# Optimization experiments

Measured on AMD Instinct MI355X. Metric: run time of the kernel, lower is better.

## Reference

```python
import jax, jax.numpy as jnp
import numpy as np

# Config (decoder-only Transformer)
NL, H, D, DK, V, B, S = 6, 16, 1024, 64, 32000, 2, 1024  # DK = d_v = D // H
DFF = 4 * D


def _layer_norm(x, g, b, eps=1e-5):
    mu = jnp.mean(x, axis=-1, keepdims=True)
    var = jnp.mean(jnp.square(x - mu), axis=-1, keepdims=True)
    return (x - mu) * jax.lax.rsqrt(var + eps) * g + b


def _pos_encoding(seq_len, d_embed):
    # Matches PositionalEncoding: base 1000 (as in source), sin at even i, cos at odd i
    pos = jnp.arange(seq_len, dtype=jnp.float32)[:, None]
    i = jnp.arange(d_embed, dtype=jnp.float32)[None, :]
    angle = pos / jnp.power(1000.0, i / d_embed)
    return jnp.where((jnp.arange(d_embed)[None, :] % 2) == 0, jnp.sin(angle), jnp.cos(angle))


def setup_inputs() -> dict:
    key = jax.random.key(0)
    ks = jax.random.split(key, 8)
    n = lambda k, shp, sc: jax.random.normal(k, shp, dtype=jnp.float32) * sc
    return {
        "outputs": jax.random.randint(ks[0], (B, S), 0, V),
        "embed": n(ks[1], (V, D), 0.02),
        # per-head Q/K/V projections stacked over layers and heads: [NL, H, D, DK]
        "Wq": n(ks[2], (NL, H, D, DK), D ** -0.5),
        "Wk": n(ks[3], (NL, H, D, DK), D ** -0.5),
        "Wv": n(ks[4], (NL, H, D, DK), D ** -0.5),
        "W1": n(ks[5], (NL, D, DFF), D ** -0.5),
        "W2": n(ks[6], (NL, DFF, D), DFF ** -0.5),
        "ln1_g": jnp.ones((NL, D), jnp.float32),
        "ln1_b": jnp.zeros((NL, D), jnp.float32),
        "ln2_g": jnp.ones((NL, D), jnp.float32),
        "ln2_b": jnp.zeros((NL, D), jnp.float32),
        "Wout": n(ks[7], (D, V), D ** -0.5),
        "bout": jnp.zeros((V,), jnp.float32),
    }


def reference(outputs, embed, Wq, Wk, Wv, W1, W2, ln1_g, ln1_b, ln2_g, ln2_b, Wout, bout):
    x = embed[outputs]                      # [B, S, D]
    x = x + _pos_encoding(S, D)
    scale = jnp.float32(DK ** 0.5)
    for l in range(NL):
        # Masked multi-head self-attention (per-head projections batched over H)
        q = jnp.einsum('bsd,hdk->bhsk', x, Wq[l])
        k = jnp.einsum('bsd,hdk->bhsk', x, Wk[l])
        v = jnp.einsum('bsd,hdk->bhsk', x, Wv[l])
        scores = jnp.einsum('bhqk,bhsk->bhqs', q, k) / scale   # [B,H,S,S]
        # Faithful to source: tril then masked_fill(score == 0, -inf)
        scores = jnp.tril(scores)
        scores = jnp.where(scores == 0, -jnp.inf, scores)
        w = jax.nn.softmax(scores, axis=-1)
        attn = jnp.einsum('bhqs,bhsv->bqhv', w, v).reshape(B, S, H * DK)
        x = _layer_norm(x + attn, ln1_g[l], ln1_b[l])
        # Position-wise FFN (dropout is identity at inference)
        h = jax.nn.relu(x @ W1[l]) @ W2[l]
        x = _layer_norm(x + h, ln2_g[l], ln2_b[l])
    return x @ Wout + bout                  # logits [B, S, V]
```

## Files before the change

### kernel.cpp

```cpp
#include <hip/hip_runtime.h>

typedef unsigned short u16;
typedef __attribute__((ext_vector_type(8))) short short8;
typedef __attribute__((ext_vector_type(4))) float f32x4;

#define NLAYER 6
#define NH 16
#define DMODEL 1024
#define DHEAD 64
#define NVOCAB 32000
#define NB 2
#define NS 1024
#define NDFF 4096
#define MTOK (NB*NS)

__device__ __forceinline__ u16 f2b(float f) {
    union { float f; unsigned u; } x; x.f = f;
    unsigned r = x.u + 0x7fffu + ((x.u >> 16) & 1u);
    return (u16)(r >> 16);
}

#define GLL16(gp, lp) __builtin_amdgcn_global_load_lds( \
    (const __attribute__((address_space(1))) void*)(gp), \
    (__attribute__((address_space(3))) void*)(lp), 16, 0, 0)

__global__ __launch_bounds__(256) void trans64(
    const float* __restrict__ src, u16* __restrict__ dst,
    int R, int C, long sStride, long dStride)
{
    __shared__ float sh[64][65];
    const int c0 = blockIdx.x * 64, r0 = blockIdx.y * 64;
    const float* s = src + (long)blockIdx.z * sStride;
    u16* d = dst + (long)blockIdx.z * dStride;
    const int tid = threadIdx.x;
    const int lr = tid >> 4, lc = (tid & 15) * 4;
    #pragma unroll
    for (int q = 0; q < 4; ++q) {
        const float4 v = *(const float4*)(s + (long)(r0 + q * 16 + lr) * C + c0 + lc);
        sh[q * 16 + lr][lc + 0] = v.x;
        sh[q * 16 + lr][lc + 1] = v.y;
        sh[q * 16 + lr][lc + 2] = v.z;
        sh[q * 16 + lr][lc + 3] = v.w;
    }
    __syncthreads();
    #pragma unroll
    for (int k = 0; k < 2; ++k) {
        const int t = tid + 256 * k;
        const int col = t >> 3, rch = (t & 7) * 8;
        u16 tmp[8];
        #pragma unroll
        for (int j = 0; j < 8; ++j) tmp[j] = f2b(sh[rch + j][col]);
        *(short8*)(d + (long)(c0 + col) * R + r0 + rch) = *(const short8*)tmp;
    }
}

__global__ void transpose_qkv(const float* __restrict__ src, u16* __restrict__ dst, int sel)
{
    __shared__ float t[32][33];
    const int bi = blockIdx.z, l = bi >> 4, h = bi & 15;
    const float* s = src + (long)bi * (DMODEL * DHEAD);
    u16* d = dst + (long)l * 3072 * DMODEL + (long)(sel * 1024 + h * 64) * DMODEL;
    const int c0 = blockIdx.x * 32, r0 = blockIdx.y * 32;
    const int tx = threadIdx.x, ty = threadIdx.y;
    #pragma unroll
    for (int j = 0; j < 32; j += 8)
        t[ty + j][tx] = s[(long)(r0 + ty + j) * DHEAD + c0 + tx];
    __syncthreads();
    #pragma unroll
    for (int j = 0; j < 32; j += 8)
        d[(long)(c0 + ty + j) * DMODEL + r0 + tx] = f2b(t[tx][ty + j]);
}

__global__ void embed_pe(const int* __restrict__ toks, const float* __restrict__ emb,
                         float* __restrict__ x, u16* __restrict__ xb)
{
    const int row = blockIdx.x;
    const int s = row & (NS - 1);
    const long erow = (long)toks[row] * DMODEL;
    const long base = (long)row * DMODEL;
    #pragma unroll
    for (int j = 0; j < 4; ++j) {
        int d = threadIdx.x + j * 256;
        float ang = (float)s * exp2f(-(float)d * (9.965784284662087f / 1024.f));
        float pe = (d & 1) ? cosf(ang) : sinf(ang);
        float v = emb[erow + d] + pe;
        x[base + d] = v;
        xb[base + d] = f2b(v);
    }
}

template<int ND>
__global__ __launch_bounds__(256) void ln_residual(
    const float* __restrict__ xin, const float* __restrict__ delta, size_t pstride,
    const float* __restrict__ g, const float* __restrict__ bb,
    float* __restrict__ xout, u16* __restrict__ xbout)
{
    __shared__ float red[8];
    const long base = (long)blockIdx.x * DMODEL;
    float v[4]; float sum = 0.f, sq = 0.f;
    #pragma unroll
    for (int j = 0; j < 4; ++j) {
        int d = threadIdx.x + j * 256;
        float t = xin[base + d];
        #pragma unroll
        for (int y = 0; y < ND; ++y) t += delta[base + (size_t)y * pstride + d];
        v[j] = t; sum += t; sq += t * t;
    }
    #pragma unroll
    for (int off = 1; off < 64; off <<= 1) {
        sum += __shfl_xor(sum, off, 64);
        sq  += __shfl_xor(sq,  off, 64);
    }
    const int wv = threadIdx.x >> 6, lane = threadIdx.x & 63;
    if (lane == 0) { red[wv] = sum; red[4 + wv] = sq; }
    __syncthreads();
    float ts = red[0] + red[1] + red[2] + red[3];
    float tq = red[4] + red[5] + red[6] + red[7];
    float mu = ts * (1.f / DMODEL);
    float var = tq * (1.f / DMODEL) - mu * mu;
    float rstd = rsqrtf(var + 1e-5f);
    #pragma unroll
    for (int j = 0; j < 4; ++j) {
        int d = threadIdx.x + j * 256;
        float y = (v[j] - mu) * rstd * g[d] + bb[d];
        xout[base + d] = y;
        xbout[base + d] = f2b(y);
    }
}

template<int BM, int EPI>
__global__ __launch_bounds__(BM*2, 2) void gemm_pipe(
    const u16* __restrict__ A, const u16* __restrict__ Bt,
    void* __restrict__ Cout, const float* __restrict__ bias,
    int M, int N, int K, int lda, int ldb, size_t zstride)
{
    constexpr int WAVES = BM / 32;
    constexpr int WC = WAVES / 2;
    constexpr int MR = BM / 32;
    constexpr int TILE = BM * 32;

    __shared__ __align__(16) u16 As[4][TILE];
    __shared__ __align__(16) u16 Bs[4][TILE];

    const int nmb = M / BM;
    const int id = blockIdx.x, nwg = gridDim.x;
    const int q = nwg >> 3, r = nwg & 7, xcd = id & 7, loc = id >> 3;
    const int swz = (xcd < r ? xcd * (q + 1) : r * (q + 1) + (xcd - r) * q) + loc;
    const int m0 = (swz % nmb) * BM, n0 = (swz / nmb) * BM;
    const int koff = blockIdx.y * K;

    const int tid = threadIdx.x, wv = tid >> 6, lane = tid & 63;
    const int wr = wv / WC, wc = wv % WC;
    const int lrow = lane & 15, ks = lane >> 4;

    const u16* gsrc[4];
    int ldso[2];
    {
        const int l4 = lane >> 2, s = lane & 3;
        #pragma unroll
        for (int j = 0; j < 2; ++j) {
            const int row = j * (WAVES * 16) + wv * 16 + l4;
            const int x = (row >> 1) & 3;
            gsrc[j]     = A  + (size_t)(m0 + row) * lda + koff + (size_t)((s ^ x) * 8);
            gsrc[2 + j] = Bt + (size_t)(n0 + row) * ldb + koff + (size_t)((s ^ x) * 8);
            ldso[j] = (j * (WAVES * 16) + wv * 16) * 32;
        }
    }
    int aoff[MR], boff[4];
    #pragma unroll
    for (int m = 0; m < MR; ++m) {
        const int row = wr * (BM / 2) + m * 16 + lrow;
        aoff[m] = row * 32 + ((ks ^ ((row >> 1) & 3)) * 8);
    }
    #pragma unroll
    for (int n = 0; n < 4; ++n) {
        const int row = wc * 64 + n * 16 + lrow;
        boff[n] = row * 32 + ((ks ^ ((row >> 1) & 3)) * 8);
    }

    const int NT = K / 32;
    auto ISSUE = [&](int t) {
        const int b = t & 3;
        const size_t ko = (size_t)t * 32;
        #pragma unroll
        for (int j = 0; j < 2; ++j) {
            GLL16(gsrc[j] + ko,     &As[b][ldso[j]]);
            GLL16(gsrc[2 + j] + ko, &Bs[b][ldso[j]]);
        }
    };

    f32x4 acc[MR][4] = {};
    ISSUE(0); ISSUE(1); ISSUE(2);

    for (int t = 0; t < NT; ++t) {
        if (t < NT - 2)       { asm volatile("s_waitcnt vmcnt(8)" ::: "memory"); }
        else if (t == NT - 2) { asm volatile("s_waitcnt vmcnt(4)" ::: "memory"); }
        else                  { asm volatile("s_waitcnt vmcnt(0)" ::: "memory"); }
        __builtin_amdgcn_sched_barrier(0);
        __builtin_amdgcn_s_barrier();
        __builtin_amdgcn_sched_barrier(0);

        const int b = t & 3;
        short8 af[MR], bf[4];
        #pragma unroll
        for (int m = 0; m < MR; ++m) af[m] = *(const short8*)(&As[b][aoff[m]]);
        #pragma unroll
        for (int n = 0; n < 4; ++n)  bf[n] = *(const short8*)(&Bs[b][boff[n]]);
        if (t + 3 < NT) ISSUE(t + 3);
        __builtin_amdgcn_s_setprio(1);
        #pragma unroll
        for (int m = 0; m < MR; ++m)
            #pragma unroll
            for (int n = 0; n < 4; ++n)
                acc[m][n] = __builtin_amdgcn_mfma_f32_16x16x32_bf16(af[m], bf[n], acc[m][n], 0, 0, 0);
        __builtin_amdgcn_s_setprio(0);
    }

    if (EPI == 0 || EPI == 3) {
        __syncthreads();
        float* patch = (float*)((BM == 256 && (wv & 4)) ? (void*)&Bs[0][0] : (void*)&As[0][0])
                       + (wv & 3) * (16 * 68);
        const int cc0 = n0 + wc * 64;
        f32x4 bvv = {};
        if (EPI == 3) bvv = *(const f32x4*)(bias + cc0 + (lane & 15) * 4);
        float* C = (float*)Cout + (EPI == 0 ? (size_t)blockIdx.y * zstride : (size_t)0);
        #pragma unroll
        for (int m = 0; m < MR; ++m) {
            #pragma unroll
            for (int n = 0; n < 4; ++n)
                #pragma unroll
                for (int i = 0; i < 4; ++i)
                    patch[(ks * 4 + i) * 68 + n * 16 + lrow] = acc[m][n][i];
            #pragma unroll
            for (int i2 = 0; i2 < 4; ++i2) {
                const int prow = i2 * 4 + ks;
                f32x4 v = *(const f32x4*)(patch + prow * 68 + (lane & 15) * 4);
                if (EPI == 3) v += bvv;
                const int rr = m0 + wr * (BM / 2) + m * 16 + prow;
                *(f32x4*)(C + (size_t)rr * N + cc0 + (lane & 15) * 4) = v;
            }
        }
    } else {
        u16* C = (u16*)Cout;
        #pragma unroll
        for (int m = 0; m < MR; ++m) {
            const int rr = m0 + wr * (BM / 2) + m * 16 + ks * 4;
            #pragma unroll
            for (int n = 0; n < 4; ++n) {
                const int cc = n0 + wc * 64 + n * 16 + lrow;
                #pragma unroll
                for (int i = 0; i < 4; ++i) {
                    float vv = acc[m][n][i];
                    if (EPI == 2) vv = fmaxf(vv, 0.f);
                    C[(size_t)(rr + i) * N + cc] = f2b(vv);
                }
            }
        }
    }
}

__global__ __launch_bounds__(256, 2) void attn_flash3(
    const u16* __restrict__ qkv, float* __restrict__ delta)
{
    __shared__ __align__(16) u16 Qs[64 * 64];
    __shared__ __align__(16) u16 Ks[64 * 64];
    __shared__ __align__(16) u16 Vts[64 * 64];
    __shared__ __align__(16) u16 Ps[4][16 * 64];

    const int pair = blockIdx.x, h = blockIdx.y, b = blockIdx.z;
    const int tid = threadIdx.x, wv = tid >> 6, lane = tid & 63;
    const int lrow = lane & 15, ks4 = lane >> 4, li4 = ks4 * 4;
    const long base = (long)b * NS * 3072;

    for (int rep = 0; rep < 2; ++rep) {
        const int qt = rep ? 15 - pair : pair;
        __syncthreads();

        #pragma unroll
        for (int i = 0; i < 2; ++i) {
            const int c = (wv * 2 + i) * 64 + lane;
            const int row = c >> 3, u = (c & 7) ^ (row & 7);
            GLL16(qkv + base + (long)(qt * 64 + row) * 3072 + h * 64 + u * 8, Qs + c * 8);
        }
        __syncthreads();
        short8 aq[2];
        {
            const int row = wv * 16 + lrow;
            aq[0] = *(const short8*)(Qs + row * 64 + ((ks4 ^ (row & 7)) * 8));
            aq[1] = *(const short8*)(Qs + row * 64 + (((4 + ks4) ^ (row & 7)) * 8));
        }

        f32x4 o[4] = {};
        float m_[4], l_[4];
        #pragma unroll
        for (int i = 0; i < 4; ++i) { m_[i] = -__builtin_inff(); l_[i] = 0.f; }

        for (int t = 0; t <= qt; ++t) {
            __syncthreads();
            #pragma unroll
            for (int i = 0; i < 2; ++i) {
                const int c = (wv * 2 + i) * 64 + lane;
                const int row = c >> 3, u = (c & 7) ^ (row & 7);
                GLL16(qkv + base + (long)(t * 64 + row) * 3072 + 1024 + h * 64 + u * 8, Ks + c * 8);
            }
            #pragma unroll
            for (int i = 0; i < 2; ++i) {
                const int c = tid + 256 * i;
                const int kv = c >> 3, d0 = (c & 7) * 8;
                short8 vv = *(const short8*)(qkv + base + (long)(t * 64 + kv) * 3072 + 2048 + h * 64 + d0);
                #pragma unroll
                for (int jj = 0; jj < 8; ++jj) {
                    const int j = jj ^ (lane & 7);
                    const int row = d0 + j;
                    Vts[row * 64 + (((kv >> 3) ^ (row & 7)) * 8) + (kv & 7)] = ((const u16*)&vv)[j];
                }
            }
            __syncthreads();

            f32x4 sa[4];
            #pragma unroll
            for (int nb = 0; nb < 4; ++nb) {
                f32x4 z = {};
                #pragma unroll
                for (int kd = 0; kd < 2; ++kd) {
                    const int row = nb * 16 + lrow;
                    short8 bk = *(const short8*)(Ks + row * 64 + (((kd * 4 + ks4) ^ (row & 7)) * 8));
                    z = __builtin_amdgcn_mfma_f32_16x16x32_bf16(aq[kd], bk, z, 0, 0, 0);
                }
                sa[nb] = z;
            }
            const int qrow0 = qt * 64 + wv * 16 + li4;
            #pragma unroll
            for (int nb = 0; nb < 4; ++nb)
                #pragma unroll
                for (int i = 0; i < 4; ++i) {
                    float sc = sa[nb][i] * 0.125f;
                    if (t == qt) {
                        int kvc = t * 64 + nb * 16 + lrow;
                        if (kvc > qrow0 + i) sc = -__builtin_inff();
                    }
                    sa[nb][i] = sc;
                }
            float mt[4];
            #pragma unroll
            for (int i = 0; i < 4; ++i)
                mt[i] = fmaxf(fmaxf(sa[0][i], sa[1][i]), fmaxf(sa[2][i], sa[3][i]));
            #pragma unroll
            for (int off = 1; off < 16; off <<= 1)
                #pragma unroll
                for (int i = 0; i < 4; ++i) mt[i] = fmaxf(mt[i], __shfl_xor(mt[i], off, 64));
            float fac[4], rs[4];
            #pragma unroll
            for (int i = 0; i < 4; ++i) {
                float mn = fmaxf(m_[i], mt[i]);
                fac[i] = expf(m_[i] - mn);
                m_[i] = mn;
                rs[i] = 0.f;
            }
            #pragma unroll
            for (int nb = 0; nb < 4; ++nb)
                #pragma unroll
                for (int i = 0; i < 4; ++i) {
                    float pp = expf(sa[nb][i] - m_[i]);
                    sa[nb][i] = pp; rs[i] += pp;
                }
            #pragma unroll
            for (int off = 1; off < 16; off <<= 1)
                #pragma unroll
                for (int i = 0; i < 4; ++i) rs[i] += __shfl_xor(rs[i], off, 64);
            #pragma unroll
            for (int i = 0; i < 4; ++i) l_[i] = l_[i] * fac[i] + rs[i];
            #pragma unroll
            for (int nd = 0; nd < 4; ++nd)
                #pragma unroll
                for (int i = 0; i < 4; ++i) o[nd][i] *= fac[i];

            u16* ps = &Ps[wv][0];
            #pragma unroll
            for (int nb = 0; nb < 4; ++nb)
                #pragma unroll
                for (int i = 0; i < 4; ++i) {
                    const int row = li4 + i, col = nb * 16 + lrow;
                    ps[row * 64 + (((col >> 3) ^ (row & 7)) * 8) + (col & 7)] = f2b(sa[nb][i]);
                }
            short8 pa[2];
            pa[0] = *(const short8*)(ps + lrow * 64 + ((ks4 ^ (lrow & 7)) * 8));
            pa[1] = *(const short8*)(ps + lrow * 64 + (((4 + ks4) ^ (lrow & 7)) * 8));
            #pragma unroll
            for (int nd = 0; nd < 4; ++nd)
                #pragma unroll
                for (int kd = 0; kd < 2; ++kd) {
                    const int row = nd * 16 + lrow;
                    short8 vb = *(const short8*)(Vts + row * 64 + (((kd * 4 + ks4) ^ (row & 7)) * 8));
                    o[nd] = __builtin_amdgcn_mfma_f32_16x16x32_bf16(pa[kd], vb, o[nd], 0, 0, 0);
                }
        }

        #pragma unroll
        for (int i = 0; i < 4; ++i) {
            const long row = (long)b * NS + qt * 64 + wv * 16 + li4 + i;
            const float inv = 1.f / l_[i];
            #pragma unroll
            for (int nd = 0; nd < 4; ++nd)
                delta[row * DMODEL + h * 64 + nd * 16 + lrow] = o[nd][i] * inv;
        }
    }
}

extern "C" void kernel_launch(void* const* d_in, const int* in_sizes, int n_in,
                              void* d_out, int out_size, void* d_ws, size_t ws_size,
                              hipStream_t stream) {
    const int*   toks  = (const int*)d_in[0];
    const float* emb   = (const float*)d_in[1];
    const float* Wq    = (const float*)d_in[2];
    const float* Wk    = (const float*)d_in[3];
    const float* Wv    = (const float*)d_in[4];
    const float* W1    = (const float*)d_in[5];
    const float* W2    = (const float*)d_in[6];
    const float* ln1g  = (const float*)d_in[7];
    const float* ln1b  = (const float*)d_in[8];
    const float* ln2g  = (const float*)d_in[9];
    const float* ln2b  = (const float*)d_in[10];
    const float* Wout  = (const float*)d_in[11];
    const float* bout  = (const float*)d_in[12];

    char* p = (char*)d_ws;
    auto alloc = [&](size_t bytes) { void* r = (void*)p; p += (bytes + 255) & ~(size_t)255; return r; };
    const size_t PSZ = (size_t)MTOK * 1024;
    u16*   Wqkv_t = (u16*)alloc((size_t)NLAYER * 3072 * 1024 * 2);
    u16*   W1t    = (u16*)alloc((size_t)NLAYER * 4096 * 1024 * 2);
    u16*   W2t    = (u16*)alloc((size_t)NLAYER * 1024 * 4096 * 2);
    u16*   Woutt  = (u16*)alloc((size_t)NVOCAB * 1024 * 2);
    float* x      = (float*)alloc((size_t)MTOK * 1024 * 4);
    u16*   xb     = (u16*)alloc((size_t)MTOK * 1024 * 2);
    u16*   qkv    = (u16*)alloc((size_t)MTOK * 3072 * 2);
    u16*   hbuf   = (u16*)alloc((size_t)MTOK * 4096 * 2);
    float* dbuf   = (float*)alloc(PSZ * 4 * 4);

    float* hbufF = (float*)hbuf;

    transpose_qkv<<<dim3(2, 32, 96), dim3(32, 8), 0, stream>>>(Wq, Wqkv_t, 0);
    transpose_qkv<<<dim3(2, 32, 96), dim3(32, 8), 0, stream>>>(Wk, Wqkv_t, 1);
    transpose_qkv<<<dim3(2, 32, 96), dim3(32, 8), 0, stream>>>(Wv, Wqkv_t, 2);
    trans64<<<dim3(64, 16, 6), 256, 0, stream>>>(W1, W1t, 1024, 4096, 1024l * 4096, 4096l * 1024);
    trans64<<<dim3(16, 64, 6), 256, 0, stream>>>(W2, W2t, 4096, 1024, 4096l * 1024, 1024l * 4096);
    trans64<<<dim3(500, 16, 1), 256, 0, stream>>>(Wout, Woutt, 1024, NVOCAB, 0, 0);

    embed_pe<<<MTOK, 256, 0, stream>>>(toks, emb, x, xb);

    for (int l = 0; l < NLAYER; ++l) {
        gemm_pipe<128, 1><<<dim3(16 * 24), 256, 0, stream>>>(
            xb, Wqkv_t + (size_t)l * 3072 * 1024, qkv, nullptr, MTOK, 3072, 1024, 1024, 1024, 0);
        attn_flash3<<<dim3(8, NH, NB), 256, 0, stream>>>(qkv, hbufF);
        ln_residual<1><<<MTOK, 256, 0, stream>>>(x, hbufF, 0,
            ln1g + l * 1024, ln1b + l * 1024, x, xb);
        gemm_pipe<128, 2><<<dim3(16 * 32), 256, 0, stream>>>(
            xb, W1t + (size_t)l * 4096 * 1024, hbuf, nullptr, MTOK, 4096, 1024, 1024, 1024, 0);
        gemm_pipe<128, 0><<<dim3(16 * 8, 4), 256, 0, stream>>>(
            hbuf, W2t + (size_t)l * 1024 * 4096, dbuf, nullptr, MTOK, 1024, 1024, 4096, 4096, PSZ);
        ln_residual<4><<<MTOK, 256, 0, stream>>>(x, dbuf, PSZ,
            ln2g + l * 1024, ln2b + l * 1024, x, xb);
    }

    gemm_pipe<128, 3><<<dim3(16 * 250), 256, 0, stream>>>(
        xb, Woutt, (float*)d_out, bout, MTOK, NVOCAB, 1024, 1024, 1024, 0);
}
```

Before: 1.288 ms.

## Double-buffer attention K/V tiles, precompute transposed V, vectorize LN, enlarge vocab GEMM tile

The QKV projection is split into a Q/K GEMM and a second GEMM that writes V already transposed, so the attention kernel can load K and V asynchronously into double-buffered LDS instead of transposing V element by element. The attention kernel uses swapped MFMA operands so each lane owns one query row, which removes most cross-lane max and sum shuffles, and it prefetches the next K/V tile during compute. The layer norm uses float4 vector loads and stores, and the final vocab projection switches to 256-row tiles with 512 threads. The cost is an extra GEMM launch per layer and higher LDS use in attention.

```diff
diff --git a/kernel.cpp b/kernel.cpp
--- a/kernel.cpp
+++ b/kernel.cpp
@@ -2,6 +2,7 @@
 
 typedef unsigned short u16;
 typedef __attribute__((ext_vector_type(8))) short short8;
+typedef __attribute__((ext_vector_type(4))) short short4_t;
 typedef __attribute__((ext_vector_type(4))) float f32x4;
 
 #define NLAYER 6
@@ -97,15 +98,13 @@
 {
     __shared__ float red[8];
     const long base = (long)blockIdx.x * DMODEL;
-    float v[4]; float sum = 0.f, sq = 0.f;
-    #pragma unroll
-    for (int j = 0; j < 4; ++j) {
-        int d = threadIdx.x + j * 256;
-        float t = xin[base + d];
-        #pragma unroll
-        for (int y = 0; y < ND; ++y) t += delta[base + (size_t)y * pstride + d];
-        v[j] = t; sum += t; sq += t * t;
-    }
+    const int d = threadIdx.x * 4;
+    f32x4 v = *(const f32x4*)(xin + base + d);
+    #pragma unroll
+    for (int y = 0; y < ND; ++y)
+        v += *(const f32x4*)(delta + base + (size_t)y * pstride + d);
+    float sum = v[0] + v[1] + v[2] + v[3];
+    float sq  = v[0]*v[0] + v[1]*v[1] + v[2]*v[2] + v[3]*v[3];
     #pragma unroll
     for (int off = 1; off < 64; off <<= 1) {
         sum += __shfl_xor(sum, off, 64);
@@ -119,13 +118,14 @@
     float mu = ts * (1.f / DMODEL);
     float var = tq * (1.f / DMODEL) - mu * mu;
     float rstd = rsqrtf(var + 1e-5f);
-    #pragma unroll
-    for (int j = 0; j < 4; ++j) {
-        int d = threadIdx.x + j * 256;
-        float y = (v[j] - mu) * rstd * g[d] + bb[d];
-        xout[base + d] = y;
-        xbout[base + d] = f2b(y);
-    }
+    const f32x4 gg = *(const f32x4*)(g + d);
+    const f32x4 bv = *(const f32x4*)(bb + d);
+    f32x4 yv = (v - mu) * rstd * gg + bv;
+    *(f32x4*)(xout + base + d) = yv;
+    u16 fourv[4];
+    #pragma unroll
+    for (int i = 0; i < 4; ++i) fourv[i] = f2b(yv[i]);
+    *(short4_t*)(xbout + base + d) = *(const short4_t*)fourv;
 }
 
 template<int BM, int EPI>
@@ -218,7 +218,7 @@
 
     if (EPI == 0 || EPI == 3) {
         __syncthreads();
-        float* patch = (float*)((BM == 256 && (wv & 4)) ? (void*)&Bs[0][0] : (void*)&As[0][0])
+        float* patch = (float*)((WAVES == 8 && (wv & 4)) ? (void*)&Bs[0][0] : (void*)&As[0][0])
                        + (wv & 3) * (16 * 68);
         const int cc0 = n0 + wc * 64;
         f32x4 bvv = {};
@@ -259,18 +259,20 @@
     }
 }
 
-__global__ __launch_bounds__(256, 2) void attn_flash3(
-    const u16* __restrict__ qkv, float* __restrict__ delta)
+__global__ __launch_bounds__(256, 2) void attn_flash4(
+    const u16* __restrict__ qk, const u16* __restrict__ vT, float* __restrict__ delta)
 {
     __shared__ __align__(16) u16 Qs[64 * 64];
-    __shared__ __align__(16) u16 Ks[64 * 64];
-    __shared__ __align__(16) u16 Vts[64 * 64];
+    __shared__ __align__(16) u16 Kd[2][64 * 64];
+    __shared__ __align__(16) u16 Vd[2][64 * 64];
     __shared__ __align__(16) u16 Ps[4][16 * 64];
 
     const int pair = blockIdx.x, h = blockIdx.y, b = blockIdx.z;
     const int tid = threadIdx.x, wv = tid >> 6, lane = tid & 63;
     const int lrow = lane & 15, ks4 = lane >> 4, li4 = ks4 * 4;
-    const long base = (long)b * NS * 3072;
+    const long baseQK = (long)b * NS * 2048;
+    const u16* vbase = vT + (long)h * 64 * 2048 + b * NS;
+    u16* ps = &Ps[wv][0];
 
     for (int rep = 0; rep < 2; ++rep) {
         const int qt = rep ? 15 - pair : pair;
@@ -280,9 +282,12 @@
         for (int i = 0; i < 2; ++i) {
             const int c = (wv * 2 + i) * 64 + lane;
             const int row = c >> 3, u = (c & 7) ^ (row & 7);
-            GLL16(qkv + base + (long)(qt * 64 + row) * 3072 + h * 64 + u * 8, Qs + c * 8);
+            GLL16(qk + baseQK + (long)(qt * 64 + row) * 2048 + h * 64 + u * 8, Qs + c * 8);
+            GLL16(qk + baseQK + (long)row * 2048 + 1024 + h * 64 + u * 8, Kd[0] + c * 8);
+            GLL16(vbase + (long)row * 2048 + u * 8, Vd[0] + c * 8);
         }
         __syncthreads();
+
         short8 aq[2];
         {
             const int row = wv * 16 + lrow;
@@ -291,32 +296,19 @@
         }
 
         f32x4 o[4] = {};
-        float m_[4], l_[4];
-        #pragma unroll
-        for (int i = 0; i < 4; ++i) { m_[i] = -__builtin_inff(); l_[i] = 0.f; }
+        float m_ = -__builtin_inff(), l_ = 0.f;
 
         for (int t = 0; t <= qt; ++t) {
-            __syncthreads();
-            #pragma unroll
-            for (int i = 0; i < 2; ++i) {
-                const int c = (wv * 2 + i) * 64 + lane;
-                const int row = c >> 3, u = (c & 7) ^ (row & 7);
-                GLL16(qkv + base + (long)(t * 64 + row) * 3072 + 1024 + h * 64 + u * 8, Ks + c * 8);
+            const int p = t & 1;
+            if (t < qt) {
+                #pragma unroll
+                for (int i = 0; i < 2; ++i) {
+                    const int c = (wv * 2 + i) * 64 + lane;
+                    const int row = c >> 3, u = (c & 7) ^ (row & 7);
+                    GLL16(qk + baseQK + (long)((t + 1) * 64 + row) * 2048 + 1024 + h * 64 + u * 8, Kd[p ^ 1] + c * 8);
+                    GLL16(vbase + (long)row * 2048 + (t + 1) * 64 + u * 8, Vd[p ^ 1] + c * 8);
+                }
             }
-            #pragma unroll
-            for (int i = 0; i < 2; ++i) {
-                const int c = tid + 256 * i;
-                const int kv = c >> 3, d0 = (c & 7) * 8;
-                short8 vv = *(const short8*)(qkv + base + (long)(t * 64 + kv) * 3072 + 2048 + h * 64 + d0);
-                #pragma unroll
-                for (int jj = 0; jj < 8; ++jj) {
-                    const int j = jj ^ (lane & 7);
-                    const int row = d0 + j;
-                    Vts[row * 64 + (((kv >> 3) ^ (row & 7)) * 8) + (kv & 7)] = ((const u16*)&vv)[j];
-                }
-            }
-            __syncthreads();
-
             f32x4 sa[4];
             #pragma unroll
             for (int nb = 0; nb < 4; ++nb) {
@@ -324,65 +316,53 @@
                 #pragma unroll
                 for (int kd = 0; kd < 2; ++kd) {
                     const int row = nb * 16 + lrow;
-                    short8 bk = *(const short8*)(Ks + row * 64 + (((kd * 4 + ks4) ^ (row & 7)) * 8));
-                    z = __builtin_amdgcn_mfma_f32_16x16x32_bf16(aq[kd], bk, z, 0, 0, 0);
+                    short8 bk = *(const short8*)(Kd[p] + row * 64 + (((kd * 4 + ks4) ^ (row & 7)) * 8));
+                    z = __builtin_amdgcn_mfma_f32_16x16x32_bf16(bk, aq[kd], z, 0, 0, 0);
                 }
                 sa[nb] = z;
             }
-            const int qrow0 = qt * 64 + wv * 16 + li4;
+            const int qg = qt * 64 + wv * 16 + lrow;
             #pragma unroll
             for (int nb = 0; nb < 4; ++nb)
                 #pragma unroll
                 for (int i = 0; i < 4; ++i) {
                     float sc = sa[nb][i] * 0.125f;
-                    if (t == qt) {
-                        int kvc = t * 64 + nb * 16 + lrow;
-                        if (kvc > qrow0 + i) sc = -__builtin_inff();
-                    }
+                    if (t == qt && (t * 64 + nb * 16 + li4 + i) > qg) sc = -__builtin_inff();
                     sa[nb][i] = sc;
                 }
-            float mt[4];
-            #pragma unroll
-            for (int i = 0; i < 4; ++i)
-                mt[i] = fmaxf(fmaxf(sa[0][i], sa[1][i]), fmaxf(sa[2][i], sa[3][i]));
-            #pragma unroll
-            for (int off = 1; off < 16; off <<= 1)
-                #pragma unroll
-                for (int i = 0; i < 4; ++i) mt[i] = fmaxf(mt[i], __shfl_xor(mt[i], off, 64));
-            float fac[4], rs[4];
-            #pragma unroll
-            for (int i = 0; i < 4; ++i) {
-                float mn = fmaxf(m_[i], mt[i]);
-                fac[i] = expf(m_[i] - mn);
-                m_[i] = mn;
-                rs[i] = 0.f;
+            float mt = sa[0][0];
+            #pragma unroll
+            for (int nb = 0; nb < 4; ++nb)
+                #pragma unroll
+                for (int i = 0; i < 4; ++i) mt = fmaxf(mt, sa[nb][i]);
+            mt = fmaxf(mt, __shfl_xor(mt, 16, 64));
+            mt = fmaxf(mt, __shfl_xor(mt, 32, 64));
+            const float mn = fmaxf(m_, mt);
+            const float fac = expf(m_ - mn);
+            m_ = mn;
+            float rs = 0.f;
+            #pragma unroll
+            for (int nb = 0; nb < 4; ++nb)
+                #pragma unroll
+                for (int i = 0; i < 4; ++i) {
+                    float pp = expf(sa[nb][i] - mn);
+                    sa[nb][i] = pp; rs += pp;
+                }
+            rs += __shfl_xor(rs, 16, 64);
+            rs += __shfl_xor(rs, 32, 64);
+            l_ = l_ * fac + rs;
+            #pragma unroll
+            for (int nd = 0; nd < 4; ++nd) o[nd] *= fac;
+
+            #pragma unroll
+            for (int nb = 0; nb < 4; ++nb) {
+                u16 fourv[4];
+                #pragma unroll
+                for (int i = 0; i < 4; ++i) fourv[i] = f2b(sa[nb][i]);
+                const int kvb = nb * 16 + li4;
+                const int addr = lrow * 64 + (((kvb >> 3) ^ (lrow & 7)) * 8) + (kvb & 7);
+                *(short4_t*)(ps + addr) = *(const short4_t*)fourv;
             }
-            #pragma unroll
-            for (int nb = 0; nb < 4; ++nb)
-                #pragma unroll
-                for (int i = 0; i < 4; ++i) {
-                    float pp = expf(sa[nb][i] - m_[i]);
-                    sa[nb][i] = pp; rs[i] += pp;
-                }
-            #pragma unroll
-            for (int off = 1; off < 16; off <<= 1)
-                #pragma unroll
-                for (int i = 0; i < 4; ++i) rs[i] += __shfl_xor(rs[i], off, 64);
-            #pragma unroll
-            for (int i = 0; i < 4; ++i) l_[i] = l_[i] * fac[i] + rs[i];
-            #pragma unroll
-            for (int nd = 0; nd < 4; ++nd)
-                #pragma unroll
-                for (int i = 0; i < 4; ++i) o[nd][i] *= fac[i];
-
-            u16* ps = &Ps[wv][0];
-            #pragma unroll
-            for (int nb = 0; nb < 4; ++nb)
-                #pragma unroll
-                for (int i = 0; i < 4; ++i) {
-                    const int row = li4 + i, col = nb * 16 + lrow;
-                    ps[row * 64 + (((col >> 3) ^ (row & 7)) * 8) + (col & 7)] = f2b(sa[nb][i]);
-                }
             short8 pa[2];
             pa[0] = *(const short8*)(ps + lrow * 64 + ((ks4 ^ (lrow & 7)) * 8));
             pa[1] = *(const short8*)(ps + lrow * 64 + (((4 + ks4) ^ (lrow & 7)) * 8));
@@ -391,18 +371,18 @@
                 #pragma unroll
                 for (int kd = 0; kd < 2; ++kd) {
                     const int row = nd * 16 + lrow;
-                    short8 vb = *(const short8*)(Vts + row * 64 + (((kd * 4 + ks4) ^ (row & 7)) * 8));
-                    o[nd] = __builtin_amdgcn_mfma_f32_16x16x32_bf16(pa[kd], vb, o[nd], 0, 0, 0);
-                }
-        }
-
-        #pragma unroll
-        for (int i = 0; i < 4; ++i) {
-            const long row = (long)b * NS + qt * 64 + wv * 16 + li4 + i;
-            const float inv = 1.f / l_[i];
-            #pragma unroll
-            for (int nd = 0; nd < 4; ++nd)
-                delta[row * DMODEL + h * 64 + nd * 16 + lrow] = o[nd][i] * inv;
+                    short8 vb = *(const short8*)(Vd[p] + row * 64 + (((kd * 4 + ks4) ^ (row & 7)) * 8));
+                    o[nd] = __builtin_amdgcn_mfma_f32_16x16x32_bf16(vb, pa[kd], o[nd], 0, 0, 0);
+                }
+            __syncthreads();
+        }
+
+        const float inv = 1.f / l_;
+        const long tok = (long)b * NS + qt * 64 + wv * 16 + lrow;
+        #pragma unroll
+        for (int nd = 0; nd < 4; ++nd) {
+            f32x4 v = o[nd] * inv;
+            *(f32x4*)(delta + tok * DMODEL + h * 64 + nd * 16 + li4) = v;
         }
     }
 }
@@ -433,7 +413,8 @@
     u16*   Woutt  = (u16*)alloc((size_t)NVOCAB * 1024 * 2);
     float* x      = (float*)alloc((size_t)MTOK * 1024 * 4);
     u16*   xb     = (u16*)alloc((size_t)MTOK * 1024 * 2);
-    u16*   qkv    = (u16*)alloc((size_t)MTOK * 3072 * 2);
+    u16*   qkbuf  = (u16*)alloc((size_t)MTOK * 2048 * 2);
+    u16*   vTbuf  = (u16*)alloc((size_t)1024 * MTOK * 2);
     u16*   hbuf   = (u16*)alloc((size_t)MTOK * 4096 * 2);
     float* dbuf   = (float*)alloc(PSZ * 4 * 4);
 
@@ -449,9 +430,12 @@
     embed_pe<<<MTOK, 256, 0, stream>>>(toks, emb, x, xb);
 
     for (int l = 0; l < NLAYER; ++l) {
-        gemm_pipe<128, 1><<<dim3(16 * 24), 256, 0, stream>>>(
-            xb, Wqkv_t + (size_t)l * 3072 * 1024, qkv, nullptr, MTOK, 3072, 1024, 1024, 1024, 0);
-        attn_flash3<<<dim3(8, NH, NB), 256, 0, stream>>>(qkv, hbufF);
+        const u16* Wl = Wqkv_t + (size_t)l * 3072 * 1024;
+        gemm_pipe<128, 1><<<dim3(16 * 16), 256, 0, stream>>>(
+            xb, Wl, qkbuf, nullptr, MTOK, 2048, 1024, 1024, 1024, 0);
+        gemm_pipe<128, 1><<<dim3(8 * 16), 256, 0, stream>>>(
+            Wl + (size_t)2048 * 1024, xb, vTbuf, nullptr, 1024, MTOK, 1024, 1024, 1024, 0);
+        attn_flash4<<<dim3(8, NH, NB), 256, 0, stream>>>(qkbuf, vTbuf, hbufF);
         ln_residual<1><<<MTOK, 256, 0, stream>>>(x, hbufF, 0,
             ln1g + l * 1024, ln1b + l * 1024, x, xb);
         gemm_pipe<128, 2><<<dim3(16 * 32), 256, 0, stream>>>(
@@ -462,6 +446,6 @@
             ln2g + l * 1024, ln2b + l * 1024, x, xb);
     }
 
-    gemm_pipe<128, 3><<<dim3(16 * 250), 256, 0, stream>>>(
+    gemm_pipe<256, 3><<<dim3(8 * 125), 512, 0, stream>>>(
         xb, Woutt, (float*)d_out, bout, MTOK, NVOCAB, 1024, 1024, 1024, 0);
 }
```

Result: faster. 1.158 ms (-10.1%).
